# Kernel tuning notes

Hardware: AMD Instinct MI355X
Metric: run time of the kernel (lower is better)

Reference implementation:

```python
import jax, jax.numpy as jnp
import numpy as np

SLOPE = 0.2  # LeakyReLU negative slope

def _mlp2(x, w1, b1, w2, b2):
    h = jax.nn.leaky_relu(x @ w1 + b1, SLOPE)
    return h @ w2 + b2

def setup_inputs() -> dict:
    key = jax.random.key(0)
    ks = jax.random.split(key, 16)
    B, N, T, A, H = 8, 512, 8, 16, 64
    D = T * A  # node_dim * timestep = 128
    s = 0.1
    return {
        "nodes": jax.random.normal(ks[0], (B, N, T, A), dtype=jnp.float32),
        "edges": jax.random.randint(ks[1], (B, N, N), 0, 2),
        "self_w1": jax.random.normal(ks[2], (D, H), dtype=jnp.float32) * s,
        "self_b1": jnp.zeros((H,), jnp.float32),
        "self_w2": jax.random.normal(ks[3], (H, H), dtype=jnp.float32) * s,
        "self_b2": jnp.zeros((H,), jnp.float32),
        "nb_w1": jax.random.normal(ks[4], (D, H), dtype=jnp.float32) * s,
        "nb_b1": jnp.zeros((H,), jnp.float32),
        "nb_w2": jax.random.normal(ks[5], (H, H), dtype=jnp.float32) * s,
        "nb_b2": jnp.zeros((H,), jnp.float32),
        "comb_w1": jax.random.normal(ks[6], (2 * H, H), dtype=jnp.float32) * s,
        "comb_b1": jnp.zeros((H,), jnp.float32),
        "comb_w2": jax.random.normal(ks[7], (H, 1), dtype=jnp.float32) * s,
        "comb_b2": jnp.zeros((1,), jnp.float32),
    }

def reference(nodes, edges, self_w1, self_b1, self_w2, self_b2,
              nb_w1, nb_b1, nb_w2, nb_b2,
              comb_w1, comb_b1, comb_w2, comb_b2):
    B, N = nodes.shape[0], nodes.shape[1]
    H = self_w2.shape[1]
    x = nodes.reshape(B, N, -1)                       # [B,N,D]
    self_e = _mlp2(x, self_w1, self_b1, self_w2, self_b2)  # [B,N,H]
    nb_e = _mlp2(x, nb_w1, nb_b1, nb_w2, nb_b2)            # [B,N,H]

    # combine_mlp(cat(self_i, nb_j)) scores; split fc1 to avoid [B,N,N,2H]
    w1_s, w1_n = comb_w1[:H], comb_w1[H:]
    pre = (jnp.einsum('bih,hk->bik', self_e, w1_s)[:, :, None, :]
           + jnp.einsum('bjh,hk->bjk', nb_e, w1_n)[:, None, :, :]
           + comb_b1)                                  # [B,N,N,H] (i=target, j=neighbor)
    scores = (jax.nn.leaky_relu(pre, SLOPE) @ comb_w2)[..., 0] + comb_b2[0]  # [B,N,N]

    # mask[b,i,j] = edges[b,j,i] != 0 and i != j
    mask = (jnp.swapaxes(edges, 1, 2) != 0) & (~jnp.eye(N, dtype=bool))
    neg = jnp.finfo(scores.dtype).min
    weights = jax.nn.softmax(jnp.where(mask, scores, neg), axis=-1)
    weights = jnp.where(mask, weights, 0.0)

    agg = jnp.einsum('bij,bjh->bih', weights, nb_e)    # weighted neighbor sum
    has_nb = mask.any(-1)                              # nodes w/o neighbors stay zero
    return jnp.where(has_nb[..., None], agg + self_e, 0.0)
```

## Files before the change

kernel.cpp:

```cpp
#include <hip/hip_runtime.h>
#include <float.h>

typedef __attribute__((ext_vector_type(8))) short short8;
typedef __attribute__((ext_vector_type(4))) float f32x4;

#define SLOPE 0.2f

__device__ __forceinline__ float leaky(float x) { return fmaxf(x, SLOPE * x); }

__device__ __forceinline__ unsigned short f2bf(float f) {
  unsigned u = __float_as_uint(f);
  return (unsigned short)((u + 0x7FFFu + ((u >> 16) & 1u)) >> 16);
}

__global__ __launch_bounds__(256) void prep(
    const float* __restrict__ nodes,
    const float* __restrict__ self_w1, const float* __restrict__ self_b1,
    const float* __restrict__ self_w2, const float* __restrict__ self_b2,
    const float* __restrict__ nb_w1,   const float* __restrict__ nb_b1,
    const float* __restrict__ nb_w2,   const float* __restrict__ nb_b2,
    const float* __restrict__ comb_w1, const float* __restrict__ comb_b1,
    const float* __restrict__ comb_w2, const float* __restrict__ comb_b2,
    float* __restrict__ self_e, float* __restrict__ ss, float* __restrict__ sn,
    float* __restrict__ sP, float* __restrict__ sQ,
    unsigned short* __restrict__ nbT)
{
  __shared__ float x_sh[8][128];
  __shared__ float h_sh[8][64];
  __shared__ float e_sh[8][64];

  const int tid = threadIdx.x, lane = tid & 63, wv = tid >> 6;
  const int node0 = blockIdx.x * 8;
  const int bb = node0 >> 9;
  const int jloc = node0 & 511;

  ((float4*)&x_sh[0][0])[tid] = ((const float4*)(nodes + (size_t)node0 * 128))[tid];
  __syncthreads();

  const int la = wv * 2, lb = la + 1;
  const float w2lane = comb_w2[lane];
  const float cb2 = comb_b2[0];
  const float cb1 = comb_b1[lane];

  for (int p = 0; p < 2; ++p) {
    const float* w1 = p ? nb_w1 : self_w1;
    const float* b1 = p ? nb_b1 : self_b1;
    const float* w2 = p ? nb_w2 : self_w2;
    const float* b2 = p ? nb_b2 : self_b2;
    const float* cw = comb_w1 + (p ? 64 * 64 : 0);

    float a0 = 0.f, a1 = 0.f, c0 = 0.f, c1 = 0.f;
    #pragma unroll 4
    for (int q = 0; q < 32; ++q) {
      float4 xa = *(const float4*)&x_sh[la][q * 4];
      float4 xb = *(const float4*)&x_sh[lb][q * 4];
      float w_0 = w1[(q * 4 + 0) * 64 + lane];
      float w_1 = w1[(q * 4 + 1) * 64 + lane];
      float w_2 = w1[(q * 4 + 2) * 64 + lane];
      float w_3 = w1[(q * 4 + 3) * 64 + lane];
      a0 += xa.x * w_0; a1 += xa.y * w_1; a0 += xa.z * w_2; a1 += xa.w * w_3;
      c0 += xb.x * w_0; c1 += xb.y * w_1; c0 += xb.z * w_2; c1 += xb.w * w_3;
    }
    {
      float bv = b1[lane];
      h_sh[la][lane] = leaky(a0 + a1 + bv);
      h_sh[lb][lane] = leaky(c0 + c1 + bv);
    }

    a0 = a1 = c0 = c1 = 0.f;
    #pragma unroll 4
    for (int q = 0; q < 16; ++q) {
      float4 ha = *(const float4*)&h_sh[la][q * 4];
      float4 hb = *(const float4*)&h_sh[lb][q * 4];
      float w_0 = w2[(q * 4 + 0) * 64 + lane];
      float w_1 = w2[(q * 4 + 1) * 64 + lane];
      float w_2 = w2[(q * 4 + 2) * 64 + lane];
      float w_3 = w2[(q * 4 + 3) * 64 + lane];
      a0 += ha.x * w_0; a1 += ha.y * w_1; a0 += ha.z * w_2; a1 += ha.w * w_3;
      c0 += hb.x * w_0; c1 += hb.y * w_1; c0 += hb.z * w_2; c1 += hb.w * w_3;
    }
    float e_a, e_b;
    {
      float bv = b2[lane];
      e_a = a0 + a1 + bv;
      e_b = c0 + c1 + bv;
    }
    e_sh[la][lane] = e_a;
    e_sh[lb][lane] = e_b;
    if (p == 0) {
      self_e[(size_t)(node0 + la) * 64 + lane] = e_a;
      self_e[(size_t)(node0 + lb) * 64 + lane] = e_b;
    }

    a0 = a1 = c0 = c1 = 0.f;
    #pragma unroll 4
    for (int q = 0; q < 16; ++q) {
      float4 ea = *(const float4*)&e_sh[la][q * 4];
      float4 eb = *(const float4*)&e_sh[lb][q * 4];
      float w_0 = cw[(q * 4 + 0) * 64 + lane];
      float w_1 = cw[(q * 4 + 1) * 64 + lane];
      float w_2 = cw[(q * 4 + 2) * 64 + lane];
      float w_3 = cw[(q * 4 + 3) * 64 + lane];
      a0 += ea.x * w_0; a1 += ea.y * w_1; a0 += ea.z * w_2; a1 += ea.w * w_3;
      c0 += eb.x * w_0; c1 += eb.y * w_1; c0 += eb.z * w_2; c1 += eb.w * w_3;
    }
    float s_a = a0 + a1 + (p ? 0.f : cb1);
    float s_b = c0 + c1 + (p ? 0.f : cb1);
    {
      float* so = p ? sn : ss;
      so[(size_t)(node0 + la) * 64 + lane] = s_a;
      so[(size_t)(node0 + lb) * 64 + lane] = s_b;
    }
    float ra = w2lane * s_a, rb = w2lane * s_b;
    #pragma unroll
    for (int off = 32; off; off >>= 1) {
      ra += __shfl_xor(ra, off);
      rb += __shfl_xor(rb, off);
    }
    if (lane == 0) {
      float* po = p ? sQ : sP;
      float add = p ? 0.f : cb2;
      po[node0 + la] = 0.6f * ra + add;
      po[node0 + lb] = 0.6f * rb + add;
    }

    if (p == 1) {
      __syncthreads();
      const int h = tid >> 2, j2 = (tid & 3) * 2;
      unsigned pack = (unsigned)f2bf(e_sh[j2][h])
                    | ((unsigned)f2bf(e_sh[j2 + 1][h]) << 16);
      *(unsigned*)(nbT + ((size_t)(bb * 64 + (jloc >> 3))) * 512 + h * 8 + j2) = pack;
    }
  }
}

__global__ __launch_bounds__(512) void gat_attn(
    const int* __restrict__ edges,
    const float* __restrict__ comb_w2,
    const float* __restrict__ self_e,
    const float* __restrict__ ss, const float* __restrict__ sn,
    const float* __restrict__ sP, const float* __restrict__ sQ,
    const unsigned short* __restrict__ nbT,
    float* __restrict__ out)
{
  __shared__ __align__(16) float sn_sh[2][64][68];
  __shared__ __align__(16) unsigned short P_sh[16][520];
  __shared__ __align__(16) float red_sh[4][64][4];
  __shared__ unsigned short jm_sh[512];
  __shared__ float f_sh[16];

  const int tid = threadIdx.x, lane = tid & 63, wv = tid >> 6;
  const int b = blockIdx.x & 7, it = blockIdx.x >> 3;
  const int i0 = it * 16;
  const size_t nodeb = (size_t)b * 512;

  const int ra = wv * 2, rb = ra + 1;
  const int ia = i0 + ra, ib = ia + 1;

  const int* eb = edges + ((size_t)(nodeb + tid)) * 512 + i0;
  const int4 ev0 = *(const int4*)(eb + 0);
  const int4 ev1 = *(const int4*)(eb + 4);
  const int4 ev2 = *(const int4*)(eb + 8);
  const int4 ev3 = *(const int4*)(eb + 12);

  float4 w2p[16], sa0[16], sa1[16];
  {
    const float4* w2v = (const float4*)comb_w2;
    const float4* s0 = (const float4*)(ss + (nodeb + ia) * 64);
    const float4* s1 = (const float4*)(ss + (nodeb + ib) * 64);
    #pragma unroll
    for (int q = 0; q < 16; ++q) {
      float4 w = w2v[q];
      w2p[q] = make_float4(0.4f * w.x, 0.4f * w.y, 0.4f * w.z, 0.4f * w.w);
      sa0[q] = s0[q];
      sa1[q] = s1[q];
    }
  }
  const float sPa = sP[nodeb + ia], sPb = sP[nodeb + ib];
  float sQv[8];
  #pragma unroll
  for (int jt = 0; jt < 8; ++jt) sQv[jt] = sQ[nodeb + jt * 64 + lane];

  {
    unsigned mj = 0;
    mj |= (ev0.x != 0 ? 1u : 0u) << 0;  mj |= (ev0.y != 0 ? 1u : 0u) << 1;
    mj |= (ev0.z != 0 ? 1u : 0u) << 2;  mj |= (ev0.w != 0 ? 1u : 0u) << 3;
    mj |= (ev1.x != 0 ? 1u : 0u) << 4;  mj |= (ev1.y != 0 ? 1u : 0u) << 5;
    mj |= (ev1.z != 0 ? 1u : 0u) << 6;  mj |= (ev1.w != 0 ? 1u : 0u) << 7;
    mj |= (ev2.x != 0 ? 1u : 0u) << 8;  mj |= (ev2.y != 0 ? 1u : 0u) << 9;
    mj |= (ev2.z != 0 ? 1u : 0u) << 10; mj |= (ev2.w != 0 ? 1u : 0u) << 11;
    mj |= (ev3.x != 0 ? 1u : 0u) << 12; mj |= (ev3.y != 0 ? 1u : 0u) << 13;
    mj |= (ev3.z != 0 ? 1u : 0u) << 14; mj |= (ev3.w != 0 ? 1u : 0u) << 15;
    const int d = tid - i0;
    if (d >= 0 && d < 16) mj &= ~(1u << d);
    jm_sh[tid] = (unsigned short)mj;
  }

  const int str = tid >> 4, stc = (tid & 15) * 4;
  const int str2 = (tid + 512) >> 4, stc2 = ((tid + 512) & 15) * 4;
  float4 st0, st1;
  {
    const float4* src = (const float4*)(sn + nodeb * 64);
    st0 = src[tid];
    st1 = src[tid + 512];
  }

  float msc0[8], msc1[8];
  int cur = 0;
  for (int jt = 0; jt < 8; ++jt) {
    *(float4*)&sn_sh[cur][str][stc] = st0;
    *(float4*)&sn_sh[cur][str2][stc2] = st1;
    if (jt < 7) {
      const float4* src = (const float4*)(sn + (nodeb + (jt + 1) * 64) * 64);
      st0 = src[tid];
      st1 = src[tid + 512];
    }
    __syncthreads();

    float acc0 = 0.f, acc1 = 0.f;
    #pragma unroll
    for (int q = 0; q < 16; ++q) {
      float4 v = *(const float4*)&sn_sh[cur][lane][q * 4];
      float4 w = w2p[q];
      float4 A = sa0[q];
      float4 Bv = sa1[q];
      acc0 += w.x * fabsf(A.x + v.x) + w.y * fabsf(A.y + v.y)
            + w.z * fabsf(A.z + v.z) + w.w * fabsf(A.w + v.w);
      acc1 += w.x * fabsf(Bv.x + v.x) + w.y * fabsf(Bv.y + v.y)
            + w.z * fabsf(Bv.z + v.z) + w.w * fabsf(Bv.w + v.w);
    }
    const unsigned mj = jm_sh[jt * 64 + lane];
    msc0[jt] = ((mj >> ra) & 1u) ? acc0 + sPa + sQv[jt] : -FLT_MAX;
    msc1[jt] = ((mj >> rb) & 1u) ? acc1 + sPb + sQv[jt] : -FLT_MAX;
    cur ^= 1;
  }

  float m0 = msc0[0], m1 = msc1[0];
  #pragma unroll
  for (int jt = 1; jt < 8; ++jt) {
    m0 = fmaxf(m0, msc0[jt]);
    m1 = fmaxf(m1, msc1[jt]);
  }
  #pragma unroll
  for (int off = 32; off; off >>= 1) {
    m0 = fmaxf(m0, __shfl_xor(m0, off));
    m1 = fmaxf(m1, __shfl_xor(m1, off));
  }

  float s0 = 0.f, s1 = 0.f;
  #pragma unroll
  for (int jt = 0; jt < 8; ++jt) {
    const float e0 = __expf(msc0[jt] - m0);
    const float e1 = __expf(msc1[jt] - m1);
    P_sh[ra][jt * 64 + lane] = f2bf(e0);
    P_sh[rb][jt * 64 + lane] = f2bf(e1);
    s0 += e0;
    s1 += e1;
  }
  #pragma unroll
  for (int off = 32; off; off >>= 1) {
    s0 += __shfl_xor(s0, off);
    s1 += __shfl_xor(s1, off);
  }
  if (lane == 0) {
    f_sh[ra] = (m0 > -1e37f) ? 1.0f / s0 : 0.0f;
    f_sh[rb] = (m1 > -1e37f) ? 1.0f / s1 : 0.0f;
  }
  __syncthreads();

  const int nt = wv & 3, kh = wv >> 2;
  const int arow = lane & 15, agrp = lane >> 4;
  const int bcol = nt * 16 + (lane & 15);
  const unsigned short* nb3 = nbT + (size_t)b * 32768 + bcol * 8;

  f32x4 C = {0.f, 0.f, 0.f, 0.f};
  #pragma unroll
  for (int ks = 0; ks < 8; ++ks) {
    const int jb = kh * 256 + ks * 32 + agrp * 8;
    short8 afr = *(const short8*)&P_sh[arow][jb];
    short8 bfr = *(const short8*)(nb3 + (size_t)jb * 64);
    C = __builtin_amdgcn_mfma_f32_16x16x32_bf16(afr, bfr, C, 0, 0, 0);
  }
  if (kh == 1) *(f32x4*)&red_sh[wv - 4][lane][0] = C;
  __syncthreads();
  if (kh == 0) {
    f32x4 P = *(const f32x4*)&red_sh[wv][lane][0];
    #pragma unroll
    for (int r = 0; r < 4; ++r) {
      const int rg = agrp * 4 + r;
      const float f = f_sh[rg];
      const size_t adr = (nodeb + i0 + rg) * 64 + bcol;
      const float val = (C[r] + P[r]) * f + self_e[adr];
      out[adr] = (f > 0.f) ? val : 0.f;
    }
  }
}

extern "C" void kernel_launch(void* const* d_in, const int* in_sizes, int n_in,
                              void* d_out, int out_size, void* d_ws, size_t ws_size,
                              hipStream_t stream) {
  const float* nodes   = (const float*)d_in[0];
  const int*   edges   = (const int*)  d_in[1];
  const float* self_w1 = (const float*)d_in[2];
  const float* self_b1 = (const float*)d_in[3];
  const float* self_w2 = (const float*)d_in[4];
  const float* self_b2 = (const float*)d_in[5];
  const float* nb_w1   = (const float*)d_in[6];
  const float* nb_b1   = (const float*)d_in[7];
  const float* nb_w2   = (const float*)d_in[8];
  const float* nb_b2   = (const float*)d_in[9];
  const float* comb_w1 = (const float*)d_in[10];
  const float* comb_b1 = (const float*)d_in[11];
  const float* comb_w2 = (const float*)d_in[12];
  const float* comb_b2 = (const float*)d_in[13];

  float* ws     = (float*)d_ws;
  float* self_e = ws;
  float* ss     = ws + 262144;
  float* sn     = ws + 524288;
  float* sP     = ws + 786432;
  float* sQ     = ws + 790528;
  unsigned short* nbT = (unsigned short*)(ws + 794624);

  prep<<<512, 256, 0, stream>>>(
      nodes, self_w1, self_b1, self_w2, self_b2,
      nb_w1, nb_b1, nb_w2, nb_b2, comb_w1, comb_b1, comb_w2, comb_b2,
      self_e, ss, sn, sP, sQ, nbT);

  gat_attn<<<256, 512, 0, stream>>>(
      edges, comb_w2, self_e, ss, sn, sP, sQ, nbT, (float*)d_out);
}
```

Baseline: 35.79 us.

## Compute node MLPs with bf16 MFMA using pre-packed weight fragments

Replaces the scalar FP32 prep kernel with two kernels. A single-block kernel converts all MLP weights into bf16 MFMA B-fragments, and a one-wave-per-16-nodes kernel runs the two MLP layers and the combine projection with 16x16x32 bf16 MFMA. This removes the per-lane scalar FMA loops and the repeated uncoalesced weight reads. It adds a kernel launch and lowers the precision of the intermediate embeddings, scores and self_e to bf16 inputs. The single-block weight prep and the 64-thread blocks may leave much of the GPU idle.

```diff
diff --git a/kernel.cpp b/kernel.cpp
--- a/kernel.cpp
+++ b/kernel.cpp
@@ -13,123 +13,188 @@
   return (unsigned short)((u + 0x7FFFu + ((u >> 16) & 1u)) >> 16);
 }
 
-__global__ __launch_bounds__(256) void prep(
+__global__ __launch_bounds__(1024) void wprep(
+    const float* __restrict__ self_w1, const float* __restrict__ self_w2,
+    const float* __restrict__ nb_w1,   const float* __restrict__ nb_w2,
+    const float* __restrict__ comb_w1,
+    unsigned short* __restrict__ wf)
+{
+  const int tid = threadIdx.x;
+  #pragma unroll
+  for (int u = 0; u < 4; ++u) {
+    const int pair = tid * 4 + u;
+    const int frag = pair >> 6, lane = pair & 63;
+    const int p = frag >> 5, fl = frag & 31;
+    const float* src;
+    int nt, kb;
+    if (fl < 16)      { src = p ? nb_w1 : self_w1; nt = fl >> 2;        kb = fl & 3; }
+    else if (fl < 24) { src = p ? nb_w2 : self_w2; nt = (fl - 16) >> 1; kb = (fl - 16) & 1; }
+    else              { src = comb_w1 + p * 4096;  nt = (fl - 24) >> 1; kb = (fl - 24) & 1; }
+    const int n = nt * 16 + (lane & 15);
+    const int k0 = kb * 32 + (lane >> 4) * 8;
+    unsigned short v[8];
+    #pragma unroll
+    for (int j = 0; j < 8; ++j) v[j] = f2bf(src[(k0 + j) * 64 + n]);
+    short8 pk;
+    #pragma unroll
+    for (int j = 0; j < 8; ++j) pk[j] = (short)v[j];
+    *(short8*)(wf + ((size_t)(frag * 64 + lane)) * 8) = pk;
+  }
+}
+
+__global__ __launch_bounds__(64) void mlp(
     const float* __restrict__ nodes,
-    const float* __restrict__ self_w1, const float* __restrict__ self_b1,
-    const float* __restrict__ self_w2, const float* __restrict__ self_b2,
-    const float* __restrict__ nb_w1,   const float* __restrict__ nb_b1,
-    const float* __restrict__ nb_w2,   const float* __restrict__ nb_b2,
-    const float* __restrict__ comb_w1, const float* __restrict__ comb_b1,
-    const float* __restrict__ comb_w2, const float* __restrict__ comb_b2,
+    const float* __restrict__ self_b1, const float* __restrict__ self_b2,
+    const float* __restrict__ nb_b1,   const float* __restrict__ nb_b2,
+    const float* __restrict__ comb_b1, const float* __restrict__ comb_w2,
+    const float* __restrict__ comb_b2,
+    const unsigned short* __restrict__ wf,
     float* __restrict__ self_e, float* __restrict__ ss, float* __restrict__ sn,
     float* __restrict__ sP, float* __restrict__ sQ,
     unsigned short* __restrict__ nbT)
 {
-  __shared__ float x_sh[8][128];
-  __shared__ float h_sh[8][64];
-  __shared__ float e_sh[8][64];
-
-  const int tid = threadIdx.x, lane = tid & 63, wv = tid >> 6;
-  const int node0 = blockIdx.x * 8;
-  const int bb = node0 >> 9;
-  const int jloc = node0 & 511;
-
-  ((float4*)&x_sh[0][0])[tid] = ((const float4*)(nodes + (size_t)node0 * 128))[tid];
-  __syncthreads();
-
-  const int la = wv * 2, lb = la + 1;
-  const float w2lane = comb_w2[lane];
+  __shared__ float tile[16][68];
+
+  const int lane = threadIdx.x;
+  const int arow = lane & 15, agrp = lane >> 4;
+  const int node0 = blockIdx.x * 16;
+  const int b = node0 >> 9, jloc = node0 & 511;
+
+  short8 xa[4];
+  {
+    const float* xrow = nodes + ((size_t)(node0 + arow)) * 128 + agrp * 8;
+    #pragma unroll
+    for (int kb = 0; kb < 4; ++kb) {
+      float v[8];
+      *(float4*)&v[0] = *(const float4*)(xrow + kb * 32);
+      *(float4*)&v[4] = *(const float4*)(xrow + kb * 32 + 4);
+      #pragma unroll
+      for (int j = 0; j < 8; ++j) xa[kb][j] = (short)f2bf(v[j]);
+    }
+  }
+
+  const float w2v = comb_w2[arow + 0 * 16];
+  float w2vn[4], cb1v[4];
+  #pragma unroll
+  for (int nt = 0; nt < 4; ++nt) {
+    w2vn[nt] = comb_w2[nt * 16 + arow];
+    cb1v[nt] = comb_b1[nt * 16 + arow];
+  }
   const float cb2 = comb_b2[0];
-  const float cb1 = comb_b1[lane];
+  (void)w2v;
 
   for (int p = 0; p < 2; ++p) {
-    const float* w1 = p ? nb_w1 : self_w1;
     const float* b1 = p ? nb_b1 : self_b1;
-    const float* w2 = p ? nb_w2 : self_w2;
     const float* b2 = p ? nb_b2 : self_b2;
-    const float* cw = comb_w1 + (p ? 64 * 64 : 0);
-
-    float a0 = 0.f, a1 = 0.f, c0 = 0.f, c1 = 0.f;
-    #pragma unroll 4
-    for (int q = 0; q < 32; ++q) {
-      float4 xa = *(const float4*)&x_sh[la][q * 4];
-      float4 xb = *(const float4*)&x_sh[lb][q * 4];
-      float w_0 = w1[(q * 4 + 0) * 64 + lane];
-      float w_1 = w1[(q * 4 + 1) * 64 + lane];
-      float w_2 = w1[(q * 4 + 2) * 64 + lane];
-      float w_3 = w1[(q * 4 + 3) * 64 + lane];
-      a0 += xa.x * w_0; a1 += xa.y * w_1; a0 += xa.z * w_2; a1 += xa.w * w_3;
-      c0 += xb.x * w_0; c1 += xb.y * w_1; c0 += xb.z * w_2; c1 += xb.w * w_3;
-    }
-    {
-      float bv = b1[lane];
-      h_sh[la][lane] = leaky(a0 + a1 + bv);
-      h_sh[lb][lane] = leaky(c0 + c1 + bv);
-    }
-
-    a0 = a1 = c0 = c1 = 0.f;
-    #pragma unroll 4
-    for (int q = 0; q < 16; ++q) {
-      float4 ha = *(const float4*)&h_sh[la][q * 4];
-      float4 hb = *(const float4*)&h_sh[lb][q * 4];
-      float w_0 = w2[(q * 4 + 0) * 64 + lane];
-      float w_1 = w2[(q * 4 + 1) * 64 + lane];
-      float w_2 = w2[(q * 4 + 2) * 64 + lane];
-      float w_3 = w2[(q * 4 + 3) * 64 + lane];
-      a0 += ha.x * w_0; a1 += ha.y * w_1; a0 += ha.z * w_2; a1 += ha.w * w_3;
-      c0 += hb.x * w_0; c1 += hb.y * w_1; c0 += hb.z * w_2; c1 += hb.w * w_3;
-    }
-    float e_a, e_b;
-    {
-      float bv = b2[lane];
-      e_a = a0 + a1 + bv;
-      e_b = c0 + c1 + bv;
-    }
-    e_sh[la][lane] = e_a;
-    e_sh[lb][lane] = e_b;
-    if (p == 0) {
-      self_e[(size_t)(node0 + la) * 64 + lane] = e_a;
-      self_e[(size_t)(node0 + lb) * 64 + lane] = e_b;
-    }
-
-    a0 = a1 = c0 = c1 = 0.f;
-    #pragma unroll 4
-    for (int q = 0; q < 16; ++q) {
-      float4 ea = *(const float4*)&e_sh[la][q * 4];
-      float4 eb = *(const float4*)&e_sh[lb][q * 4];
-      float w_0 = cw[(q * 4 + 0) * 64 + lane];
-      float w_1 = cw[(q * 4 + 1) * 64 + lane];
-      float w_2 = cw[(q * 4 + 2) * 64 + lane];
-      float w_3 = cw[(q * 4 + 3) * 64 + lane];
-      a0 += ea.x * w_0; a1 += ea.y * w_1; a0 += ea.z * w_2; a1 += ea.w * w_3;
-      c0 += eb.x * w_0; c1 += eb.y * w_1; c0 += eb.z * w_2; c1 += eb.w * w_3;
-    }
-    float s_a = a0 + a1 + (p ? 0.f : cb1);
-    float s_b = c0 + c1 + (p ? 0.f : cb1);
-    {
-      float* so = p ? sn : ss;
-      so[(size_t)(node0 + la) * 64 + lane] = s_a;
-      so[(size_t)(node0 + lb) * 64 + lane] = s_b;
-    }
-    float ra = w2lane * s_a, rb = w2lane * s_b;
-    #pragma unroll
-    for (int off = 32; off; off >>= 1) {
-      ra += __shfl_xor(ra, off);
-      rb += __shfl_xor(rb, off);
-    }
-    if (lane == 0) {
+    const unsigned short* wfp = wf + (size_t)p * 32 * 64 * 8;
+
+    short8 w1f[16], w2f[8], cwf[8];
+    #pragma unroll
+    for (int i = 0; i < 16; ++i)
+      w1f[i] = *(const short8*)(wfp + ((size_t)(i * 64 + lane)) * 8);
+    #pragma unroll
+    for (int i = 0; i < 8; ++i)
+      w2f[i] = *(const short8*)(wfp + ((size_t)((16 + i) * 64 + lane)) * 8);
+    #pragma unroll
+    for (int i = 0; i < 8; ++i)
+      cwf[i] = *(const short8*)(wfp + ((size_t)((24 + i) * 64 + lane)) * 8);
+
+    f32x4 acc[4];
+    #pragma unroll
+    for (int nt = 0; nt < 4; ++nt) acc[nt] = (f32x4){0.f, 0.f, 0.f, 0.f};
+    #pragma unroll
+    for (int kb = 0; kb < 4; ++kb)
+      #pragma unroll
+      for (int nt = 0; nt < 4; ++nt)
+        acc[nt] = __builtin_amdgcn_mfma_f32_16x16x32_bf16(xa[kb], w1f[nt * 4 + kb], acc[nt], 0, 0, 0);
+    #pragma unroll
+    for (int nt = 0; nt < 4; ++nt) {
+      const float bv = b1[nt * 16 + arow];
+      #pragma unroll
+      for (int r = 0; r < 4; ++r)
+        tile[agrp * 4 + r][nt * 16 + arow] = leaky(acc[nt][r] + bv);
+    }
+
+    short8 ha[2];
+    #pragma unroll
+    for (int kb = 0; kb < 2; ++kb) {
+      float v[8];
+      *(float4*)&v[0] = *(const float4*)&tile[arow][kb * 32 + agrp * 8];
+      *(float4*)&v[4] = *(const float4*)&tile[arow][kb * 32 + agrp * 8 + 4];
+      #pragma unroll
+      for (int j = 0; j < 8; ++j) ha[kb][j] = (short)f2bf(v[j]);
+    }
+
+    #pragma unroll
+    for (int nt = 0; nt < 4; ++nt) acc[nt] = (f32x4){0.f, 0.f, 0.f, 0.f};
+    #pragma unroll
+    for (int kb = 0; kb < 2; ++kb)
+      #pragma unroll
+      for (int nt = 0; nt < 4; ++nt)
+        acc[nt] = __builtin_amdgcn_mfma_f32_16x16x32_bf16(ha[kb], w2f[nt * 2 + kb], acc[nt], 0, 0, 0);
+    #pragma unroll
+    for (int nt = 0; nt < 4; ++nt) {
+      const float bv = b2[nt * 16 + arow];
+      #pragma unroll
+      for (int r = 0; r < 4; ++r) {
+        const float ev = acc[nt][r] + bv;
+        tile[agrp * 4 + r][nt * 16 + arow] = ev;
+        if (p == 0)
+          self_e[((size_t)(node0 + agrp * 4 + r)) * 64 + nt * 16 + arow] = ev;
+      }
+    }
+
+    short8 ea[2];
+    #pragma unroll
+    for (int kb = 0; kb < 2; ++kb) {
+      float v[8];
+      *(float4*)&v[0] = *(const float4*)&tile[arow][kb * 32 + agrp * 8];
+      *(float4*)&v[4] = *(const float4*)&tile[arow][kb * 32 + agrp * 8 + 4];
+      #pragma unroll
+      for (int j = 0; j < 8; ++j) ea[kb][j] = (short)f2bf(v[j]);
+    }
+
+    if (p == 1) {
+      #pragma unroll
+      for (int g = 0; g < 2; ++g) {
+        short8 pk;
+        #pragma unroll
+        for (int jj = 0; jj < 8; ++jj)
+          pk[jj] = (short)f2bf(tile[g * 8 + jj][lane]);
+        *(short8*)(nbT + (size_t)b * 32768 + ((size_t)((jloc >> 3) + g)) * 512 + lane * 8) = pk;
+      }
+    }
+
+    #pragma unroll
+    for (int nt = 0; nt < 4; ++nt) acc[nt] = (f32x4){0.f, 0.f, 0.f, 0.f};
+    #pragma unroll
+    for (int kb = 0; kb < 2; ++kb)
+      #pragma unroll
+      for (int nt = 0; nt < 4; ++nt)
+        acc[nt] = __builtin_amdgcn_mfma_f32_16x16x32_bf16(ea[kb], cwf[nt * 2 + kb], acc[nt], 0, 0, 0);
+
+    float* so = p ? sn : ss;
+    float t[4] = {0.f, 0.f, 0.f, 0.f};
+    #pragma unroll
+    for (int nt = 0; nt < 4; ++nt) {
+      #pragma unroll
+      for (int r = 0; r < 4; ++r) {
+        const float sv = acc[nt][r] + (p ? 0.f : cb1v[nt]);
+        so[((size_t)(node0 + agrp * 4 + r)) * 64 + nt * 16 + arow] = sv;
+        t[r] += w2vn[nt] * sv;
+      }
+    }
+    #pragma unroll
+    for (int r = 0; r < 4; ++r) {
+      #pragma unroll
+      for (int off = 1; off < 16; off <<= 1) t[r] += __shfl_xor(t[r], off);
+    }
+    if (arow == 0) {
       float* po = p ? sQ : sP;
-      float add = p ? 0.f : cb2;
-      po[node0 + la] = 0.6f * ra + add;
-      po[node0 + lb] = 0.6f * rb + add;
-    }
-
-    if (p == 1) {
-      __syncthreads();
-      const int h = tid >> 2, j2 = (tid & 3) * 2;
-      unsigned pack = (unsigned)f2bf(e_sh[j2][h])
-                    | ((unsigned)f2bf(e_sh[j2 + 1][h]) << 16);
-      *(unsigned*)(nbT + ((size_t)(bb * 64 + (jloc >> 3))) * 512 + h * 8 + j2) = pack;
+      const float add = p ? 0.f : cb2;
+      #pragma unroll
+      for (int r = 0; r < 4; ++r)
+        po[node0 + agrp * 4 + r] = 0.6f * t[r] + add;
     }
   }
 }
@@ -157,11 +222,11 @@
   const int ra = wv * 2, rb = ra + 1;
   const int ia = i0 + ra, ib = ia + 1;
 
-  const int* eb = edges + ((size_t)(nodeb + tid)) * 512 + i0;
-  const int4 ev0 = *(const int4*)(eb + 0);
-  const int4 ev1 = *(const int4*)(eb + 4);
-  const int4 ev2 = *(const int4*)(eb + 8);
-  const int4 ev3 = *(const int4*)(eb + 12);
+  const int* ebp = edges + ((size_t)(nodeb + tid)) * 512 + i0;
+  const int4 ev0 = *(const int4*)(ebp + 0);
+  const int4 ev1 = *(const int4*)(ebp + 4);
+  const int4 ev2 = *(const int4*)(ebp + 8);
+  const int4 ev3 = *(const int4*)(ebp + 12);
 
   float4 w2p[16], sa0[16], sa1[16];
   {
@@ -321,11 +386,13 @@
   float* sP     = ws + 786432;
   float* sQ     = ws + 790528;
   unsigned short* nbT = (unsigned short*)(ws + 794624);
-
-  prep<<<512, 256, 0, stream>>>(
-      nodes, self_w1, self_b1, self_w2, self_b2,
-      nb_w1, nb_b1, nb_w2, nb_b2, comb_w1, comb_b1, comb_w2, comb_b2,
-      self_e, ss, sn, sP, sQ, nbT);
+  unsigned short* wf  = (unsigned short*)(ws + 925696);
+
+  wprep<<<1, 1024, 0, stream>>>(self_w1, self_w2, nb_w1, nb_w2, comb_w1, wf);
+
+  mlp<<<256, 64, 0, stream>>>(
+      nodes, self_b1, self_b2, nb_b1, nb_b2, comb_b1, comb_w2, comb_b2,
+      wf, self_e, ss, sn, sP, sQ, nbT);
 
   gat_attn<<<256, 512, 0, stream>>>(
       edges, comb_w2, self_e, ss, sn, sP, sQ, nbT, (float*)d_out);
```

New measurement: 34.47 us. -3.7%, faster.
